# Kernel tuning notes

Measured on AMD Instinct MI355X. Metric: run time of the kernel, lower is better.

Reference implementation:

```python
import jax, jax.numpy as jnp
import numpy as np

N_NODES = 100000
N_EDGES = 6400000
D_IN = 512
D_HID = 16
N_CLASSES = 16


def setup_inputs() -> dict:
    key = jax.random.key(0)
    k1, k2, k3, k4, k5, k6 = jax.random.split(key, 6)
    x = jax.random.normal(k1, (N_NODES, D_IN), dtype=jnp.float32)
    edge_index = jax.random.randint(k2, (2, N_EDGES), 0, N_NODES, dtype=jnp.int64)
    # Glorot-style init for GCN weights
    W1 = jax.random.normal(k3, (D_IN, D_HID), dtype=jnp.float32) * (1.0 / np.sqrt(D_IN))
    b1 = jnp.zeros((D_HID,), dtype=jnp.float32)
    W2 = jax.random.normal(k4, (D_HID, N_CLASSES), dtype=jnp.float32) * (1.0 / np.sqrt(D_HID))
    b2 = jnp.zeros((N_CLASSES,), dtype=jnp.float32)
    return {"x": x, "W1": W1, "b1": b1, "W2": W2, "b2": b2, "edge_index": edge_index}


def reference(x, W1, b1, W2, b2, edge_index):
    N = x.shape[0]
    loops = jnp.arange(N, dtype=edge_index.dtype)
    # GCN: add self-loops, symmetric D^-1/2 A D^-1/2 normalization
    src = jnp.concatenate([edge_index[0], loops])  # [E+N]
    dst = jnp.concatenate([edge_index[1], loops])  # [E+N]
    deg = jax.ops.segment_sum(jnp.ones(src.shape[0], dtype=x.dtype), dst, num_segments=N)
    dinv = jnp.where(deg > 0, jax.lax.rsqrt(deg), 0.0)
    norm = (dinv[src] * dinv[dst])[:, None]  # [E+N, 1]

    def gcn_conv(h, W, b):
        h = h @ W                                  # [N, d_out] transform first (PyG order)
        agg = jax.ops.segment_sum(h[src] * norm, dst, num_segments=N)
        return agg + b

    h = jax.nn.relu(gcn_conv(x, W1, b1))
    # F.dropout(training=self.training) is identity in eval mode
    logits = gcn_conv(h, W2, b2)
    return jax.nn.log_softmax(logits, axis=1)
```

## Files before the change

kernel.cpp:

```cpp
#include <hip/hip_runtime.h>
#include <hip/hip_bf16.h>
#include <math.h>

#define N_NODES 100000
#define N_EDGES 6400000
#define D_IN 512
#define D_HID 16

#define NBKT 782
#define NBP  784
#define NBLK 1000
#define EPB  6400

__global__ __launch_bounds__(256) void khist(const int* __restrict__ dst,
                                             int* __restrict__ hist_mat) {
    __shared__ int h[NBP];
    int tid = threadIdx.x;
    int blk = blockIdx.x;
    for (int i = tid; i < NBP; i += 256) h[i] = 0;
    __syncthreads();
    int base = blk * EPB;
#pragma unroll
    for (int k = 0; k < 25; k++)
        atomicAdd(&h[dst[base + k * 256 + tid] >> 7], 1);
    __syncthreads();
    for (int i = tid; i < NBKT; i += 256) hist_mat[blk * NBP + i] = h[i];
}

__global__ __launch_bounds__(256) void kbtot(const int* __restrict__ hist_mat,
                                             int* __restrict__ btot) {
    __shared__ int sd[256];
    int b = blockIdx.x;
    int t = threadIdx.x;
    int s = 0;
    for (int r = t; r < NBLK; r += 256) s += hist_mat[r * NBP + b];
    sd[t] = s;
    __syncthreads();
    for (int off = 128; off > 0; off >>= 1) {
        if (t < off) sd[t] += sd[t + off];
        __syncthreads();
    }
    if (t == 0) btot[b] = sd[0];
}

__global__ __launch_bounds__(1024) void kbscan(const int* __restrict__ btot,
                                               int* __restrict__ bbase) {
    __shared__ int sd[1024];
    int t = threadIdx.x;
    int v = (t < NBKT) ? btot[t] : 0;
    sd[t] = v;
    __syncthreads();
    for (int off = 1; off < 1024; off <<= 1) {
        int u = (t >= off) ? sd[t - off] : 0;
        __syncthreads();
        sd[t] += u;
        __syncthreads();
    }
    if (t < NBKT) bbase[t] = sd[t] - v;
}

__global__ __launch_bounds__(256) void kbase(const int* __restrict__ hist_mat,
                                             const int* __restrict__ bbase,
                                             int* __restrict__ base_mat) {
    __shared__ int sd[256];
    __shared__ int chunk_tot;
    int b = blockIdx.x;
    int t = threadIdx.x;
    int running = bbase[b];
    for (int c0 = 0; c0 < NBLK; c0 += 256) {
        int r = c0 + t;
        int v = (r < NBLK) ? hist_mat[r * NBP + b] : 0;
        sd[t] = v;
        __syncthreads();
        for (int off = 1; off < 256; off <<= 1) {
            int u = (t >= off) ? sd[t - off] : 0;
            __syncthreads();
            sd[t] += u;
            __syncthreads();
        }
        if (r < NBLK) base_mat[r * NBP + b] = running + sd[t] - v;
        if (t == 255) chunk_tot = sd[255];
        __syncthreads();
        running += chunk_tot;
        __syncthreads();
    }
}

__global__ __launch_bounds__(256) void kscatter(const int* __restrict__ src,
                                                const int* __restrict__ dst,
                                                const int* __restrict__ base_mat,
                                                unsigned int* __restrict__ ebuf) {
    __shared__ int cur[NBP];
    int tid = threadIdx.x;
    int blk = blockIdx.x;
    for (int i = tid; i < NBKT; i += 256) cur[i] = base_mat[blk * NBP + i];
    __syncthreads();
    int base = blk * EPB;
#pragma unroll 4
    for (int k = 0; k < 25; k++) {
        int e = base + k * 256 + tid;
        int d = dst[e];
        int s = src[e];
        int p = atomicAdd(&cur[d >> 7], 1);
        ebuf[p] = ((unsigned int)s << 7) | (unsigned int)(d & 127);
    }
}

__global__ __launch_bounds__(256) void kdeg(const unsigned int* __restrict__ ebuf,
                                            const int* __restrict__ btot,
                                            const int* __restrict__ bbase,
                                            float* __restrict__ dinv) {
    __shared__ int h[128];
    int t = threadIdx.x;
    int b = blockIdx.x;
    if (t < 128) h[t] = 0;
    __syncthreads();
    int cnt = btot[b];
    int start = bbase[b];
    for (int i = t; i < cnt; i += 256)
        atomicAdd(&h[ebuf[start + i] & 127u], 1);
    __syncthreads();
    if (t < 128) {
        int node = b * 128 + t;
        if (node < N_NODES) dinv[node] = rsqrtf((float)h[t] + 1.0f);
    }
}

__global__ __launch_bounds__(256) void gemm1(const float* __restrict__ x,
                                             const float* __restrict__ W1,
                                             const float* __restrict__ dinv,
                                             float* __restrict__ h1p) {
    __shared__ float xs[256 * 33];
    int tid = threadIdx.x;
    int row0 = blockIdx.x * 256;
    int row = row0 + tid;
    float acc[16];
#pragma unroll
    for (int c = 0; c < 16; c++) acc[c] = 0.f;

    for (int k0 = 0; k0 < D_IN; k0 += 32) {
        __syncthreads();
#pragma unroll
        for (int l = 0; l < 8; l++) {
            int idx = tid + l * 256;
            int r = idx >> 3;
            int f4 = idx & 7;
            int gr = row0 + r;
            float4 v = make_float4(0.f, 0.f, 0.f, 0.f);
            if (gr < N_NODES)
                v = *(const float4*)(x + (size_t)gr * D_IN + k0 + f4 * 4);
            int a = r * 33 + f4 * 4;
            xs[a] = v.x; xs[a + 1] = v.y; xs[a + 2] = v.z; xs[a + 3] = v.w;
        }
        __syncthreads();
#pragma unroll
        for (int kk = 0; kk < 32; kk++) {
            float xv = xs[tid * 33 + kk];
            const float* wr = W1 + (k0 + kk) * 16;
#pragma unroll
            for (int c = 0; c < 16; c++) acc[c] = fmaf(xv, wr[c], acc[c]);
        }
    }
    if (row < N_NODES) {
        float di = dinv[row];
        float4* o = (float4*)(h1p + (size_t)row * 16);
        o[0] = make_float4(acc[0] * di, acc[1] * di, acc[2] * di, acc[3] * di);
        o[1] = make_float4(acc[4] * di, acc[5] * di, acc[6] * di, acc[7] * di);
        o[2] = make_float4(acc[8] * di, acc[9] * di, acc[10] * di, acc[11] * di);
        o[3] = make_float4(acc[12] * di, acc[13] * di, acc[14] * di, acc[15] * di);
    }
}

__global__ __launch_bounds__(512) void kagg1(const float* __restrict__ h1p,
                                             const float* __restrict__ dinv,
                                             const unsigned int* __restrict__ ebuf,
                                             const int* __restrict__ btot,
                                             const int* __restrict__ bbase,
                                             const float* __restrict__ b1,
                                             const float* __restrict__ W2,
                                             float* __restrict__ h3p) {
    __shared__ float acc[128 * 16];
    __shared__ float dinvb[128];
    __shared__ float w2s[256];
    __shared__ float b1s[16];
    int t = threadIdx.x;
    int b = blockIdx.x;
    int nb0 = b * 128;
    if (t < 128) {
        int n = nb0 + t;
        dinvb[t] = (n < N_NODES) ? dinv[n] : 0.f;
    }
    if (t >= 128 && t < 384) w2s[t - 128] = W2[t - 128];
    if (t >= 384 && t < 400) b1s[t - 384] = b1[t - 384];
    for (int idx = t; idx < 2048; idx += 512) {
        int n = nb0 + (idx >> 4);
        acc[idx] = (n < N_NODES) ? h1p[(size_t)n * 16 + (idx & 15)] : 0.f;
    }
    __syncthreads();
    int cnt = btot[b];
    int start = bbase[b];
    int c = t & 15;
    for (int i = (t >> 4); i < cnt; i += 32) {
        unsigned int e = ebuf[start + i];
        float v = h1p[(size_t)(e >> 7) * 16 + c];
        unsafeAtomicAdd(&acc[(e & 127u) * 16 + c], v);
    }
    __syncthreads();
    for (int idx = t; idx < 2048; idx += 512) {
        int node = idx >> 4;
        int cc = idx & 15;
        int gn = nb0 + node;
        if (gn >= N_NODES) continue;
        float di = dinvb[node];
        float out = 0.f;
#pragma unroll
        for (int j = 0; j < 16; j++) {
            float u = fmaf(di, acc[node * 16 + j], b1s[j]);
            u = u > 0.f ? u : 0.f;
            out = fmaf(u, w2s[j * 16 + cc], out);
        }
        h3p[(size_t)gn * 16 + cc] = out * di;
    }
}

__global__ __launch_bounds__(512) void kagg2(const float* __restrict__ h3p,
                                             const float* __restrict__ dinv,
                                             const unsigned int* __restrict__ ebuf,
                                             const int* __restrict__ btot,
                                             const int* __restrict__ bbase,
                                             const float* __restrict__ b2,
                                             float* __restrict__ out) {
    __shared__ float acc[128 * 16];
    __shared__ float dinvb[128];
    __shared__ float b2s[16];
    int t = threadIdx.x;
    int b = blockIdx.x;
    int nb0 = b * 128;
    if (t < 128) {
        int n = nb0 + t;
        dinvb[t] = (n < N_NODES) ? dinv[n] : 0.f;
    }
    if (t >= 128 && t < 144) b2s[t - 128] = b2[t - 128];
    for (int idx = t; idx < 2048; idx += 512) {
        int n = nb0 + (idx >> 4);
        acc[idx] = (n < N_NODES) ? h3p[(size_t)n * 16 + (idx & 15)] : 0.f;
    }
    __syncthreads();
    int cnt = btot[b];
    int start = bbase[b];
    int c = t & 15;
    for (int i = (t >> 4); i < cnt; i += 32) {
        unsigned int e = ebuf[start + i];
        float v = h3p[(size_t)(e >> 7) * 16 + c];
        unsafeAtomicAdd(&acc[(e & 127u) * 16 + c], v);
    }
    __syncthreads();
    int grp = t >> 4;
#pragma unroll
    for (int rep = 0; rep < 4; rep++) {
        int node = grp + rep * 32;
        int gn = nb0 + node;
        float di = dinvb[node];
        float logit = fmaf(di, acc[node * 16 + c], b2s[c]);
        float m = logit;
#pragma unroll
        for (int mask = 1; mask < 16; mask <<= 1)
            m = fmaxf(m, __shfl_xor(m, mask, 16));
        float e = expf(logit - m);
        float ssum = e;
#pragma unroll
        for (int mask = 1; mask < 16; mask <<= 1)
            ssum += __shfl_xor(ssum, mask, 16);
        if (gn < N_NODES)
            out[(size_t)gn * 16 + c] = (logit - m) - logf(ssum);
    }
}

extern "C" void kernel_launch(void* const* d_in, const int* in_sizes, int n_in,
                              void* d_out, int out_size, void* d_ws, size_t ws_size,
                              hipStream_t stream) {
    const float* x  = (const float*)d_in[0];
    const float* W1 = (const float*)d_in[1];
    const float* b1 = (const float*)d_in[2];
    const float* W2 = (const float*)d_in[3];
    const float* b2 = (const float*)d_in[4];
    const int*   ei = (const int*)d_in[5];
    const int* src = ei;
    const int* dst = ei + N_EDGES;
    float* out = (float*)d_out;

    int* hist_mat  = (int*)d_ws;
    int* base_mat  = hist_mat + NBLK * NBP;
    int* btot      = base_mat + NBLK * NBP;
    int* bbase     = btot + 1024;
    float* dinv    = (float*)(bbase + 1024);
    unsigned int* ebuf = (unsigned int*)(dinv + 100352);
    float* h1p     = (float*)(ebuf + N_EDGES);
    float* h3p     = h1p + 1600000;

    khist<<<NBLK, 256, 0, stream>>>(dst, hist_mat);
    kbtot<<<NBKT, 256, 0, stream>>>(hist_mat, btot);
    kbscan<<<1, 1024, 0, stream>>>(btot, bbase);
    kbase<<<NBKT, 256, 0, stream>>>(hist_mat, bbase, base_mat);
    kscatter<<<NBLK, 256, 0, stream>>>(src, dst, base_mat, ebuf);
    kdeg<<<NBKT, 256, 0, stream>>>(ebuf, btot, bbase, dinv);
    gemm1<<<(N_NODES + 255) / 256, 256, 0, stream>>>(x, W1, dinv, h1p);
    kagg1<<<NBKT, 512, 0, stream>>>(h1p, dinv, ebuf, btot, bbase, b1, W2, h3p);
    kagg2<<<NBKT, 512, 0, stream>>>(h3p, dinv, ebuf, btot, bbase, b2, out);
}
```

Measured before the change: 1.898 ms.

## Store hidden features as fp16, coarsen edge bucketing, unroll aggregation gathers

Hidden feature buffers h1p and h3p are now stored in half precision, which halves the bytes moved by the random per-edge gathers in both aggregation kernels. The histogram and scatter passes use 250 blocks of 25600 edges instead of 1000 blocks, so the per-bucket scans fit in one 256-thread pass without a chunk loop. The aggregation kernels move to 256 threads and unroll the gather loop four ways to keep more independent loads in flight. fp16 storage adds rounding error to intermediate features, and fewer scatter blocks may reduce parallelism in the histogram and scatter phases.

After: 1.879 ms. Within noise of the previous version (-1.0%).

```diff
diff --git a/kernel.cpp b/kernel.cpp
--- a/kernel.cpp
+++ b/kernel.cpp
@@ -1,5 +1,6 @@
 #include <hip/hip_runtime.h>
 #include <hip/hip_bf16.h>
+#include <hip/hip_fp16.h>
 #include <math.h>
 
 #define N_NODES 100000
@@ -9,8 +10,8 @@
 
 #define NBKT 782
 #define NBP  784
-#define NBLK 1000
-#define EPB  6400
+#define NBLK 250
+#define EPB  25600
 
 __global__ __launch_bounds__(256) void khist(const int* __restrict__ dst,
                                              int* __restrict__ hist_mat) {
@@ -20,8 +21,8 @@
     for (int i = tid; i < NBP; i += 256) h[i] = 0;
     __syncthreads();
     int base = blk * EPB;
-#pragma unroll
-    for (int k = 0; k < 25; k++)
+#pragma unroll 4
+    for (int k = 0; k < 100; k++)
         atomicAdd(&h[dst[base + k * 256 + tid] >> 7], 1);
     __syncthreads();
     for (int i = tid; i < NBKT; i += 256) hist_mat[blk * NBP + i] = h[i];
@@ -32,8 +33,7 @@
     __shared__ int sd[256];
     int b = blockIdx.x;
     int t = threadIdx.x;
-    int s = 0;
-    for (int r = t; r < NBLK; r += 256) s += hist_mat[r * NBP + b];
+    int s = (t < NBLK) ? hist_mat[t * NBP + b] : 0;
     sd[t] = s;
     __syncthreads();
     for (int off = 128; off > 0; off >>= 1) {
@@ -63,27 +63,18 @@
                                              const int* __restrict__ bbase,
                                              int* __restrict__ base_mat) {
     __shared__ int sd[256];
-    __shared__ int chunk_tot;
-    int b = blockIdx.x;
-    int t = threadIdx.x;
-    int running = bbase[b];
-    for (int c0 = 0; c0 < NBLK; c0 += 256) {
-        int r = c0 + t;
-        int v = (r < NBLK) ? hist_mat[r * NBP + b] : 0;
-        sd[t] = v;
-        __syncthreads();
-        for (int off = 1; off < 256; off <<= 1) {
-            int u = (t >= off) ? sd[t - off] : 0;
-            __syncthreads();
-            sd[t] += u;
-            __syncthreads();
-        }
-        if (r < NBLK) base_mat[r * NBP + b] = running + sd[t] - v;
-        if (t == 255) chunk_tot = sd[255];
-        __syncthreads();
-        running += chunk_tot;
-        __syncthreads();
-    }
+    int b = blockIdx.x;
+    int t = threadIdx.x;
+    int v = (t < NBLK) ? hist_mat[t * NBP + b] : 0;
+    sd[t] = v;
+    __syncthreads();
+    for (int off = 1; off < 256; off <<= 1) {
+        int u = (t >= off) ? sd[t - off] : 0;
+        __syncthreads();
+        sd[t] += u;
+        __syncthreads();
+    }
+    if (t < NBLK) base_mat[t * NBP + b] = bbase[b] + sd[t] - v;
 }
 
 __global__ __launch_bounds__(256) void kscatter(const int* __restrict__ src,
@@ -97,7 +88,7 @@
     __syncthreads();
     int base = blk * EPB;
 #pragma unroll 4
-    for (int k = 0; k < 25; k++) {
+    for (int k = 0; k < 100; k++) {
         int e = base + k * 256 + tid;
         int d = dst[e];
         int s = src[e];
@@ -129,7 +120,7 @@
 __global__ __launch_bounds__(256) void gemm1(const float* __restrict__ x,
                                              const float* __restrict__ W1,
                                              const float* __restrict__ dinv,
-                                             float* __restrict__ h1p) {
+                                             __half* __restrict__ h1p16) {
     __shared__ float xs[256 * 33];
     int tid = threadIdx.x;
     int row0 = blockIdx.x * 256;
@@ -163,22 +154,23 @@
     }
     if (row < N_NODES) {
         float di = dinv[row];
-        float4* o = (float4*)(h1p + (size_t)row * 16);
-        o[0] = make_float4(acc[0] * di, acc[1] * di, acc[2] * di, acc[3] * di);
-        o[1] = make_float4(acc[4] * di, acc[5] * di, acc[6] * di, acc[7] * di);
-        o[2] = make_float4(acc[8] * di, acc[9] * di, acc[10] * di, acc[11] * di);
-        o[3] = make_float4(acc[12] * di, acc[13] * di, acc[14] * di, acc[15] * di);
-    }
-}
-
-__global__ __launch_bounds__(512) void kagg1(const float* __restrict__ h1p,
+        alignas(16) __half hv[16];
+#pragma unroll
+        for (int c = 0; c < 16; c++) hv[c] = __float2half(acc[c] * di);
+        uint4* o = (uint4*)(h1p16 + (size_t)row * 16);
+        o[0] = *(uint4*)hv;
+        o[1] = *(uint4*)(hv + 8);
+    }
+}
+
+__global__ __launch_bounds__(256) void kagg1(const __half* __restrict__ h1p16,
                                              const float* __restrict__ dinv,
                                              const unsigned int* __restrict__ ebuf,
                                              const int* __restrict__ btot,
                                              const int* __restrict__ bbase,
                                              const float* __restrict__ b1,
                                              const float* __restrict__ W2,
-                                             float* __restrict__ h3p) {
+                                             __half* __restrict__ h3p16) {
     __shared__ float acc[128 * 16];
     __shared__ float dinvb[128];
     __shared__ float w2s[256];
@@ -190,25 +182,41 @@
         int n = nb0 + t;
         dinvb[t] = (n < N_NODES) ? dinv[n] : 0.f;
     }
-    if (t >= 128 && t < 384) w2s[t - 128] = W2[t - 128];
-    if (t >= 384 && t < 400) b1s[t - 384] = b1[t - 384];
-    for (int idx = t; idx < 2048; idx += 512) {
+    w2s[t] = W2[t];
+    if (t < 16) b1s[t] = b1[t];
+    for (int idx = t; idx < 2048; idx += 256) {
         int n = nb0 + (idx >> 4);
-        acc[idx] = (n < N_NODES) ? h1p[(size_t)n * 16 + (idx & 15)] : 0.f;
+        acc[idx] = (n < N_NODES) ? __half2float(h1p16[(size_t)n * 16 + (idx & 15)]) : 0.f;
     }
     __syncthreads();
     int cnt = btot[b];
     int start = bbase[b];
+    int g = t >> 4;
     int c = t & 15;
-    for (int i = (t >> 4); i < cnt; i += 32) {
+    int i = g;
+    for (; i + 48 < cnt; i += 64) {
+        unsigned int e0 = ebuf[start + i];
+        unsigned int e1 = ebuf[start + i + 16];
+        unsigned int e2 = ebuf[start + i + 32];
+        unsigned int e3 = ebuf[start + i + 48];
+        float v0 = __half2float(h1p16[(size_t)(e0 >> 7) * 16 + c]);
+        float v1 = __half2float(h1p16[(size_t)(e1 >> 7) * 16 + c]);
+        float v2 = __half2float(h1p16[(size_t)(e2 >> 7) * 16 + c]);
+        float v3 = __half2float(h1p16[(size_t)(e3 >> 7) * 16 + c]);
+        atomicAdd(&acc[(e0 & 127u) * 16 + c], v0);
+        atomicAdd(&acc[(e1 & 127u) * 16 + c], v1);
+        atomicAdd(&acc[(e2 & 127u) * 16 + c], v2);
+        atomicAdd(&acc[(e3 & 127u) * 16 + c], v3);
+    }
+    for (; i < cnt; i += 16) {
         unsigned int e = ebuf[start + i];
-        float v = h1p[(size_t)(e >> 7) * 16 + c];
-        unsafeAtomicAdd(&acc[(e & 127u) * 16 + c], v);
-    }
-    __syncthreads();
-    for (int idx = t; idx < 2048; idx += 512) {
-        int node = idx >> 4;
-        int cc = idx & 15;
+        float v = __half2float(h1p16[(size_t)(e >> 7) * 16 + c]);
+        atomicAdd(&acc[(e & 127u) * 16 + c], v);
+    }
+    __syncthreads();
+#pragma unroll
+    for (int r = 0; r < 8; r++) {
+        int node = r * 16 + g;
         int gn = nb0 + node;
         if (gn >= N_NODES) continue;
         float di = dinvb[node];
@@ -217,13 +225,13 @@
         for (int j = 0; j < 16; j++) {
             float u = fmaf(di, acc[node * 16 + j], b1s[j]);
             u = u > 0.f ? u : 0.f;
-            out = fmaf(u, w2s[j * 16 + cc], out);
+            out = fmaf(u, w2s[j * 16 + c], out);
         }
-        h3p[(size_t)gn * 16 + cc] = out * di;
-    }
-}
-
-__global__ __launch_bounds__(512) void kagg2(const float* __restrict__ h3p,
+        h3p16[(size_t)gn * 16 + c] = __float2half(out * di);
+    }
+}
+
+__global__ __launch_bounds__(256) void kagg2(const __half* __restrict__ h3p16,
                                              const float* __restrict__ dinv,
                                              const unsigned int* __restrict__ ebuf,
                                              const int* __restrict__ btot,
@@ -240,25 +248,40 @@
         int n = nb0 + t;
         dinvb[t] = (n < N_NODES) ? dinv[n] : 0.f;
     }
-    if (t >= 128 && t < 144) b2s[t - 128] = b2[t - 128];
-    for (int idx = t; idx < 2048; idx += 512) {
+    if (t < 16) b2s[t] = b2[t];
+    for (int idx = t; idx < 2048; idx += 256) {
         int n = nb0 + (idx >> 4);
-        acc[idx] = (n < N_NODES) ? h3p[(size_t)n * 16 + (idx & 15)] : 0.f;
+        acc[idx] = (n < N_NODES) ? __half2float(h3p16[(size_t)n * 16 + (idx & 15)]) : 0.f;
     }
     __syncthreads();
     int cnt = btot[b];
     int start = bbase[b];
+    int g = t >> 4;
     int c = t & 15;
-    for (int i = (t >> 4); i < cnt; i += 32) {
+    int i = g;
+    for (; i + 48 < cnt; i += 64) {
+        unsigned int e0 = ebuf[start + i];
+        unsigned int e1 = ebuf[start + i + 16];
+        unsigned int e2 = ebuf[start + i + 32];
+        unsigned int e3 = ebuf[start + i + 48];
+        float v0 = __half2float(h3p16[(size_t)(e0 >> 7) * 16 + c]);
+        float v1 = __half2float(h3p16[(size_t)(e1 >> 7) * 16 + c]);
+        float v2 = __half2float(h3p16[(size_t)(e2 >> 7) * 16 + c]);
+        float v3 = __half2float(h3p16[(size_t)(e3 >> 7) * 16 + c]);
+        atomicAdd(&acc[(e0 & 127u) * 16 + c], v0);
+        atomicAdd(&acc[(e1 & 127u) * 16 + c], v1);
+        atomicAdd(&acc[(e2 & 127u) * 16 + c], v2);
+        atomicAdd(&acc[(e3 & 127u) * 16 + c], v3);
+    }
+    for (; i < cnt; i += 16) {
         unsigned int e = ebuf[start + i];
-        float v = h3p[(size_t)(e >> 7) * 16 + c];
-        unsafeAtomicAdd(&acc[(e & 127u) * 16 + c], v);
-    }
-    __syncthreads();
-    int grp = t >> 4;
-#pragma unroll
-    for (int rep = 0; rep < 4; rep++) {
-        int node = grp + rep * 32;
+        float v = __half2float(h3p16[(size_t)(e >> 7) * 16 + c]);
+        atomicAdd(&acc[(e & 127u) * 16 + c], v);
+    }
+    __syncthreads();
+#pragma unroll
+    for (int r = 0; r < 8; r++) {
+        int node = r * 16 + g;
         int gn = nb0 + node;
         float di = dinvb[node];
         float logit = fmaf(di, acc[node * 16 + c], b2s[c]);
@@ -295,8 +318,8 @@
     int* bbase     = btot + 1024;
     float* dinv    = (float*)(bbase + 1024);
     unsigned int* ebuf = (unsigned int*)(dinv + 100352);
-    float* h1p     = (float*)(ebuf + N_EDGES);
-    float* h3p     = h1p + 1600000;
+    __half* h1p16  = (__half*)(ebuf + N_EDGES);
+    __half* h3p16  = h1p16 + 1605632;
 
     khist<<<NBLK, 256, 0, stream>>>(dst, hist_mat);
     kbtot<<<NBKT, 256, 0, stream>>>(hist_mat, btot);
@@ -304,7 +327,7 @@
     kbase<<<NBKT, 256, 0, stream>>>(hist_mat, bbase, base_mat);
     kscatter<<<NBLK, 256, 0, stream>>>(src, dst, base_mat, ebuf);
     kdeg<<<NBKT, 256, 0, stream>>>(ebuf, btot, bbase, dinv);
-    gemm1<<<(N_NODES + 255) / 256, 256, 0, stream>>>(x, W1, dinv, h1p);
-    kagg1<<<NBKT, 512, 0, stream>>>(h1p, dinv, ebuf, btot, bbase, b1, W2, h3p);
-    kagg2<<<NBKT, 512, 0, stream>>>(h3p, dinv, ebuf, btot, bbase, b2, out);
-}
+    gemm1<<<(N_NODES + 255) / 256, 256, 0, stream>>>(x, W1, dinv, h1p16);
+    kagg1<<<NBKT, 256, 0, stream>>>(h1p16, dinv, ebuf, btot, bbase, b1, W2, h3p16);
+    kagg2<<<NBKT, 256, 0, stream>>>(h3p16, dinv, ebuf, btot, bbase, b2, out);
+}
```
